# Optimization experiments

Measured on AMD Instinct MI355X. Metric: run time of the kernel, lower is better.

The kernel has to match this reference:

```python
import jax, jax.numpy as jnp
import numpy as np

N, E, D, H = 50000, 1600000, 256, 256
EPS = 1e-5

def prelu(x, a):
    return jnp.where(x >= 0, x, a * x)

def batch_norm(x, gamma, beta):
    # training-mode BatchNorm1d: stats over the node (batch) dim
    mu = jnp.mean(x, axis=0)
    var = jnp.var(x, axis=0)
    return (x - mu) * jax.lax.rsqrt(var + EPS) * gamma + beta

def gcn_conv(x, edge_index, W, b):
    # PyG GCNConv: h = XW, add self-loops, symmetric norm, scatter-add, + bias
    h = x @ W
    n = x.shape[0]
    row = jnp.concatenate([edge_index[0], jnp.arange(n)])
    col = jnp.concatenate([edge_index[1], jnp.arange(n)])
    w = jnp.ones(row.shape[0], dtype=x.dtype)
    deg = jax.ops.segment_sum(w, col, num_segments=n)
    dinv = jnp.where(deg > 0, jax.lax.rsqrt(deg), 0.0)
    norm = dinv[row] * w * dinv[col]  # [E+N]
    msg = h[row] * norm[:, None]      # [E+N, H] gathered messages
    out = jax.ops.segment_sum(msg, col, num_segments=n)
    return out + b

def setup_inputs() -> dict:
    key = jax.random.key(0)
    ks = jax.random.split(key, 10)
    x = jax.random.normal(ks[0], (N, D), dtype=jnp.float32)
    edge_index = jax.random.randint(ks[1], (2, E), 0, N).astype(jnp.int64)
    s1 = 1.0 / np.sqrt(D)
    s2 = 1.0 / np.sqrt(H)
    return {
        "x": x,
        "edge_index": edge_index,
        "W1": jax.random.uniform(ks[2], (D, H), jnp.float32, -s1, s1),
        "b1": jnp.zeros((H,), jnp.float32),
        "W2": jax.random.uniform(ks[3], (H, H), jnp.float32, -s2, s2),
        "b2": jnp.zeros((H,), jnp.float32),
        "prelu_a": jnp.asarray(0.25, jnp.float32),
        "bn_gamma": jnp.ones((H,), jnp.float32),
        "bn_beta": jnp.zeros((H,), jnp.float32),
        "proj_W": jax.random.uniform(ks[4], (H, H), jnp.float32, -s2, s2),
        "proj_b": jnp.zeros((H,), jnp.float32),
        "pbn_gamma": jnp.ones((H,), jnp.float32),
        "pbn_beta": jnp.zeros((H,), jnp.float32),
        "prelu2_a": jnp.asarray(0.25, jnp.float32),
    }

def reference(x, edge_index, W1, b1, W2, b2, prelu_a, bn_gamma, bn_beta,
              proj_W, proj_b, pbn_gamma, pbn_beta, prelu2_a):
    # eval-mode dropout (identity); BN uses batch stats
    z = prelu(gcn_conv(x, edge_index, W1, b1), prelu_a)
    z = prelu(gcn_conv(z, edge_index, W2, b2), prelu_a)
    z = batch_norm(z, bn_gamma, bn_beta)
    p = prelu(batch_norm(z @ proj_W + proj_b, pbn_gamma, pbn_beta), prelu2_a)
    return (z, p)
```

## Files before the change

kernel.cpp:

```cpp
#include <hip/hip_runtime.h>
#include <hip/hip_bf16.h>


#define CAP 96

typedef __attribute__((ext_vector_type(8))) short short8;
typedef __attribute__((ext_vector_type(4))) float f32x4;

__device__ __forceinline__ float bf2f(unsigned short u) {
    union { unsigned int i; float f; } v; v.i = ((unsigned int)u) << 16; return v.f;
}
__device__ __forceinline__ unsigned short f2bf(float f) {
    __hip_bfloat16 h = __float2bfloat16(f);
    return *reinterpret_cast<unsigned short*>(&h);
}

__global__ __launch_bounds__(256) void k_init(float* deg, int* fill, float* stats, int N) {
    int i = blockIdx.x * 256 + threadIdx.x;
    if (i < N) { deg[i] = 1.0f; fill[i] = 0; }
    if (i < 2048) stats[i] = 0.0f;
}

__global__ __launch_bounds__(256) void k_count(const int* __restrict__ col, float* __restrict__ deg, int E) {
    int e = blockIdx.x * 256 + threadIdx.x;
    if (e < E) atomicAdd(&deg[col[e]], 1.0f);
}

__global__ __launch_bounds__(256) void k_dinv(float* deg, int N) {
    int i = blockIdx.x * 256 + threadIdx.x;
    if (i < N) deg[i] = rsqrtf(deg[i]);
}

__global__ __launch_bounds__(256) void k_fill(const int* __restrict__ row, const int* __restrict__ col,
                                              int* __restrict__ fill, int* __restrict__ csr, int E) {
    int e = blockIdx.x * 256 + threadIdx.x;
    if (e >= E) return;
    int v = col[e];
    int p = atomicAdd(&fill[v], 1);
    if (p < CAP) csr[(size_t)v * CAP + p] = row[e];
}

__global__ __launch_bounds__(256) void k_castx(const float* __restrict__ x, unsigned short* __restrict__ xb, size_t n4) {
    size_t stride = (size_t)gridDim.x * blockDim.x;
    for (size_t i = (size_t)blockIdx.x * blockDim.x + threadIdx.x; i < n4; i += stride) {
        float4 v = ((const float4*)x)[i];
        ushort4 o; o.x = f2bf(v.x); o.y = f2bf(v.y); o.z = f2bf(v.z); o.w = f2bf(v.w);
        ((ushort4*)xb)[i] = o;
    }
}

__global__ __launch_bounds__(256) void k_wt(const float* __restrict__ W, unsigned short* __restrict__ Wt) {
    __shared__ float t[32][33];
    int bx = blockIdx.x * 32, by = blockIdx.y * 32;
    int x = threadIdx.x & 31, y = threadIdx.x >> 5;
#pragma unroll
    for (int i = 0; i < 32; i += 8)
        t[y + i][x] = W[(size_t)(by + y + i) * 256 + bx + x];
    __syncthreads();
#pragma unroll
    for (int i = 0; i < 32; i += 8)
        Wt[(size_t)(bx + y + i) * 256 + by + x] = f2bf(t[x][y + i]);
}

__global__ __launch_bounds__(256) void k_gemm_bf16(const unsigned short* __restrict__ A,
                                                   const unsigned short* __restrict__ Bt,
                                                   unsigned short* __restrict__ C, int M) {
    __shared__ unsigned short As[128 * 64];
    __shared__ unsigned short Bs[128 * 64];
    int tid  = threadIdx.x;
    int lane = tid & 63, wid = tid >> 6;
    int wr = wid >> 1, wc = wid & 1;
    int row0 = blockIdx.x * 128;
    int col0 = blockIdx.y * 128;

    f32x4 acc[4][4];
#pragma unroll
    for (int m = 0; m < 4; ++m)
#pragma unroll
        for (int n = 0; n < 4; ++n) acc[m][n] = f32x4{0.f, 0.f, 0.f, 0.f};

    int srow = lane >> 3;
    int sk   = (lane & 7) * 8;

    for (int k0 = 0; k0 < 256; k0 += 64) {
#pragma unroll
        for (int i = 0; i < 4; ++i) {
            int u = i * 4 + wid;
            int arow = row0 + u * 8 + srow;
            if (arow >= M) arow = M - 1;
            const unsigned short* ga = A  + (size_t)arow * 256 + k0 + sk;
            const unsigned short* gb = Bt + (size_t)(col0 + u * 8 + srow) * 256 + k0 + sk;
            __builtin_amdgcn_global_load_lds((const __attribute__((address_space(1))) void*)ga,
                (__attribute__((address_space(3))) void*)(As + u * 512), 16, 0, 0);
            __builtin_amdgcn_global_load_lds((const __attribute__((address_space(1))) void*)gb,
                (__attribute__((address_space(3))) void*)(Bs + u * 512), 16, 0, 0);
        }
        __syncthreads();
#pragma unroll
        for (int kk = 0; kk < 64; kk += 32) {
            short8 a[4], b[4];
#pragma unroll
            for (int m = 0; m < 4; ++m)
                a[m] = *(const short8*)(As + (wr * 64 + m * 16 + (lane & 15)) * 64 + kk + (lane >> 4) * 8);
#pragma unroll
            for (int n = 0; n < 4; ++n)
                b[n] = *(const short8*)(Bs + (wc * 64 + n * 16 + (lane & 15)) * 64 + kk + (lane >> 4) * 8);
#pragma unroll
            for (int m = 0; m < 4; ++m)
#pragma unroll
                for (int n = 0; n < 4; ++n)
                    acc[m][n] = __builtin_amdgcn_mfma_f32_16x16x32_bf16(a[m], b[n], acc[m][n], 0, 0, 0);
        }
        __syncthreads();
    }

    int crow = row0 + wr * 64;
    int ccol = col0 + wc * 64;
#pragma unroll
    for (int m = 0; m < 4; ++m)
#pragma unroll
        for (int r = 0; r < 4; ++r) {
            int rr = crow + m * 16 + (lane >> 4) * 4 + r;
            if (rr < M) {
#pragma unroll
                for (int n = 0; n < 4; ++n)
                    C[(size_t)rr * 256 + ccol + n * 16 + (lane & 15)] = f2bf(acc[m][n][r]);
            }
        }
}

__global__ __launch_bounds__(256) void k_agg_bf(const unsigned short* __restrict__ h,
                                                unsigned short* __restrict__ outb,
                                                const float* __restrict__ dinv, const int* __restrict__ csr,
                                                const int* __restrict__ fill, const float* __restrict__ bias,
                                                const float* __restrict__ aptr, int N) {
    int wv = threadIdx.x >> 6, lane = threadIdx.x & 63;
    int v = blockIdx.x * 4 + wv;
    if (v >= N) return;
    const ushort4* h4 = (const ushort4*)h;
    float dv = dinv[v];
    ushort4 hv = h4[(size_t)v * 64 + lane];
    float s0 = dv * bf2f(hv.x), s1 = dv * bf2f(hv.y), s2 = dv * bf2f(hv.z), s3 = dv * bf2f(hv.w);
    int n = fill[v]; if (n > CAP) n = CAP;
    const int* lst = csr + (size_t)v * CAP;
    int i = 0;
    for (; i + 3 < n; i += 4) {
        int u0 = lst[i], u1 = lst[i + 1], u2 = lst[i + 2], u3 = lst[i + 3];
        ushort4 a0 = h4[(size_t)u0 * 64 + lane];
        ushort4 a1 = h4[(size_t)u1 * 64 + lane];
        ushort4 a2 = h4[(size_t)u2 * 64 + lane];
        ushort4 a3 = h4[(size_t)u3 * 64 + lane];
        float d0 = dinv[u0], d1 = dinv[u1], d2 = dinv[u2], d3 = dinv[u3];
        s0 += d0 * bf2f(a0.x) + d1 * bf2f(a1.x) + d2 * bf2f(a2.x) + d3 * bf2f(a3.x);
        s1 += d0 * bf2f(a0.y) + d1 * bf2f(a1.y) + d2 * bf2f(a2.y) + d3 * bf2f(a3.y);
        s2 += d0 * bf2f(a0.z) + d1 * bf2f(a1.z) + d2 * bf2f(a2.z) + d3 * bf2f(a3.z);
        s3 += d0 * bf2f(a0.w) + d1 * bf2f(a1.w) + d2 * bf2f(a2.w) + d3 * bf2f(a3.w);
    }
    for (; i < n; ++i) {
        int u0 = lst[i];
        ushort4 a0 = h4[(size_t)u0 * 64 + lane];
        float d0 = dinv[u0];
        s0 += d0 * bf2f(a0.x); s1 += d0 * bf2f(a0.y); s2 += d0 * bf2f(a0.z); s3 += d0 * bf2f(a0.w);
    }
    float a = *aptr;
    float4 bb = *(const float4*)(bias + lane * 4);
    float o0 = dv * s0 + bb.x, o1 = dv * s1 + bb.y, o2 = dv * s2 + bb.z, o3 = dv * s3 + bb.w;
    o0 = o0 >= 0.f ? o0 : a * o0;
    o1 = o1 >= 0.f ? o1 : a * o1;
    o2 = o2 >= 0.f ? o2 : a * o2;
    o3 = o3 >= 0.f ? o3 : a * o3;
    ushort4 o; o.x = f2bf(o0); o.y = f2bf(o1); o.z = f2bf(o2); o.w = f2bf(o3);
    ((ushort4*)outb)[(size_t)v * 64 + lane] = o;
}

__global__ __launch_bounds__(256) void k_bnstats_bf(const unsigned short* __restrict__ X, float* __restrict__ sums, int N) {
    int c = threadIdx.x;
    float s = 0.f, q = 0.f;
    for (int r = blockIdx.x; r < N; r += gridDim.x) {
        float x = bf2f(X[(size_t)r * 256 + c]);
        s += x; q += x * x;
    }
    atomicAdd(&sums[c], s);
    atomicAdd(&sums[256 + c], q);
}

__global__ __launch_bounds__(256) void k_bnfinal(float* stats, const float* __restrict__ gamma,
                                                 const float* __restrict__ beta, float invN) {
    int c = threadIdx.x;
    float mu = stats[c] * invN;
    float var = stats[256 + c] * invN - mu * mu;
    float rstd = rsqrtf(var + 1e-5f);
    float sc = rstd * gamma[c];
    stats[512 + c] = sc;
    stats[768 + c] = beta[c] - mu * sc;
}

__global__ __launch_bounds__(256) void k_bnapply_z(const unsigned short* __restrict__ in,
                                                   float* __restrict__ zout, unsigned short* __restrict__ zb,
                                                   const float* __restrict__ scale, const float* __restrict__ shift,
                                                   size_t n4) {
    size_t stride = (size_t)gridDim.x * blockDim.x;
    for (size_t i = (size_t)blockIdx.x * blockDim.x + threadIdx.x; i < n4; i += stride) {
        int c4 = (int)(i & 63) * 4;
        ushort4 x4 = ((const ushort4*)in)[i];
        float4 sc = *(const float4*)(scale + c4);
        float4 sh = *(const float4*)(shift + c4);
        float4 y;
        y.x = bf2f(x4.x) * sc.x + sh.x;
        y.y = bf2f(x4.y) * sc.y + sh.y;
        y.z = bf2f(x4.z) * sc.z + sh.z;
        y.w = bf2f(x4.w) * sc.w + sh.w;
        ((float4*)zout)[i] = y;
        ushort4 o; o.x = f2bf(y.x); o.y = f2bf(y.y); o.z = f2bf(y.z); o.w = f2bf(y.w);
        ((ushort4*)zb)[i] = o;
    }
}

__global__ __launch_bounds__(256) void k_bnapply_p(const unsigned short* __restrict__ in,
                                                   float* __restrict__ pout,
                                                   const float* __restrict__ scale, const float* __restrict__ shift,
                                                   const float* __restrict__ aptr, size_t n4) {
    size_t stride = (size_t)gridDim.x * blockDim.x;
    float a = *aptr;
    for (size_t i = (size_t)blockIdx.x * blockDim.x + threadIdx.x; i < n4; i += stride) {
        int c4 = (int)(i & 63) * 4;
        ushort4 x4 = ((const ushort4*)in)[i];
        float4 sc = *(const float4*)(scale + c4);
        float4 sh = *(const float4*)(shift + c4);
        float4 y;
        y.x = bf2f(x4.x) * sc.x + sh.x;
        y.y = bf2f(x4.y) * sc.y + sh.y;
        y.z = bf2f(x4.z) * sc.z + sh.z;
        y.w = bf2f(x4.w) * sc.w + sh.w;
        y.x = y.x >= 0.f ? y.x : a * y.x;
        y.y = y.y >= 0.f ? y.y : a * y.y;
        y.z = y.z >= 0.f ? y.z : a * y.z;
        y.w = y.w >= 0.f ? y.w : a * y.w;
        ((float4*)pout)[i] = y;
    }
}

extern "C" void kernel_launch(void* const* d_in, const int* in_sizes, int n_in,
                              void* d_out, int out_size, void* d_ws, size_t ws_size,
                              hipStream_t stream) {
    const float* x     = (const float*)d_in[0];
    const int*   ei    = (const int*)d_in[1];
    const float* W1    = (const float*)d_in[2];
    const float* b1    = (const float*)d_in[3];
    const float* W2    = (const float*)d_in[4];
    const float* b2    = (const float*)d_in[5];
    const float* aptr  = (const float*)d_in[6];
    const float* gamma = (const float*)d_in[7];
    const float* beta  = (const float*)d_in[8];
    const float* projW = (const float*)d_in[9];
    const float* pgamma = (const float*)d_in[11];
    const float* pbeta  = (const float*)d_in[12];
    const float* a2ptr  = (const float*)d_in[13];

    int N = in_sizes[0] / 256;
    int E = in_sizes[1] / 2;
    const int* row = ei;
    const int* col = ei + E;

    float* out  = (float*)d_out;
    float* zout = out;
    float* pout = out + (size_t)N * 256;

    unsigned short* B0 = (unsigned short*)d_ws;
    unsigned short* B1 = B0 + (size_t)N * 256;
    unsigned short* B2 = B1 + (size_t)N * 256;
    unsigned short* Wt = B2 + (size_t)N * 256;
    float* deg   = (float*)(Wt + 3 * 65536);
    int*   fill  = (int*)(deg + N);
    int*   csr   = fill + N;
    float* stats = (float*)(csr + (size_t)N * CAP);

    int nb_N = (N + 255) / 256;
    int nb_E = (E + 255) / 256;
    dim3 ggrid((N + 127) / 128, 2);
    dim3 wgrid(8, 8);
    int  agrid = (N + 3) / 4;
    size_t n4 = (size_t)N * 64;

    k_init <<<nb_N, 256, 0, stream>>>(deg, fill, stats, N);
    k_count<<<nb_E, 256, 0, stream>>>(col, deg, E);
    k_dinv <<<nb_N, 256, 0, stream>>>(deg, N);
    k_fill <<<nb_E, 256, 0, stream>>>(row, col, fill, csr, E);
    k_castx<<<2048, 256, 0, stream>>>(x, B0, n4);
    k_wt   <<<wgrid, 256, 0, stream>>>(W1,    Wt);
    k_wt   <<<wgrid, 256, 0, stream>>>(W2,    Wt + 65536);
    k_wt   <<<wgrid, 256, 0, stream>>>(projW, Wt + 131072);

    k_gemm_bf16<<<ggrid, 256, 0, stream>>>(B0, Wt, B1, N);
    k_agg_bf   <<<agrid, 256, 0, stream>>>(B1, B2, deg, csr, fill, b1, aptr, N);
    k_gemm_bf16<<<ggrid, 256, 0, stream>>>(B2, Wt + 65536, B1, N);
    k_agg_bf   <<<agrid, 256, 0, stream>>>(B1, B0, deg, csr, fill, b2, aptr, N);
    k_bnstats_bf<<<500, 256, 0, stream>>>(B0, stats, N);
    k_bnfinal   <<<1, 256, 0, stream>>>(stats, gamma, beta, 1.0f / (float)N);
    k_bnapply_z <<<2048, 256, 0, stream>>>(B0, zout, B2, stats + 512, stats + 768, n4);
    k_gemm_bf16 <<<ggrid, 256, 0, stream>>>(B2, Wt + 131072, B1, N);
    k_bnstats_bf<<<500, 256, 0, stream>>>(B1, stats + 1024, N);
    k_bnfinal   <<<1, 256, 0, stream>>>(stats + 1024, pgamma, pbeta, 1.0f / (float)N);
    k_bnapply_p <<<2048, 256, 0, stream>>>(B1, pout, stats + 1536, stats + 1792, a2ptr, n4);
}
```

Baseline: 757.4 us.

## Build CSR via two-level binning with shared-memory atomics; pad neighbor lists

Replaces the degree-count, rsqrt and global-atomic CSR fill kernels with a binning pass that groups edges into 128-node buckets split across 8 partitions. A per-bucket kernel then scatters them into the CSR using shared-memory atomics and computes dinv directly. Neighbor lists are padded to multiples of 8 with a sentinel node whose dinv is zero, so the aggregation loop is unrolled by 8 and has no remainder loop. BN stats are vectorized to ushort4 per lane. The cost is fixed per-segment capacity limits (SEGCAP) that could drop edges on skewed graphs, and bins reuse the B1 buffer.

```diff
diff --git a/kernel.cpp b/kernel.cpp
--- a/kernel.cpp
+++ b/kernel.cpp
@@ -3,6 +3,9 @@
 
 
 #define CAP 96
+#define NPB 128
+#define NPART 8
+#define SEGCAP 768
 
 typedef __attribute__((ext_vector_type(8))) short short8;
 typedef __attribute__((ext_vector_type(4))) float f32x4;
@@ -15,29 +18,57 @@
     return *reinterpret_cast<unsigned short*>(&h);
 }
 
-__global__ __launch_bounds__(256) void k_init(float* deg, int* fill, float* stats, int N) {
+__global__ __launch_bounds__(256) void k_zero(int* segcnt, int nseg, float* stats, float* dinv, int N) {
     int i = blockIdx.x * 256 + threadIdx.x;
-    if (i < N) { deg[i] = 1.0f; fill[i] = 0; }
+    if (i < nseg) segcnt[i] = 0;
     if (i < 2048) stats[i] = 0.0f;
-}
-
-__global__ __launch_bounds__(256) void k_count(const int* __restrict__ col, float* __restrict__ deg, int E) {
-    int e = blockIdx.x * 256 + threadIdx.x;
-    if (e < E) atomicAdd(&deg[col[e]], 1.0f);
-}
-
-__global__ __launch_bounds__(256) void k_dinv(float* deg, int N) {
-    int i = blockIdx.x * 256 + threadIdx.x;
-    if (i < N) deg[i] = rsqrtf(deg[i]);
-}
-
-__global__ __launch_bounds__(256) void k_fill(const int* __restrict__ row, const int* __restrict__ col,
-                                              int* __restrict__ fill, int* __restrict__ csr, int E) {
+    if (i == 0) dinv[N] = 0.0f;
+}
+
+__global__ __launch_bounds__(256) void k_bin(const int* __restrict__ row, const int* __restrict__ col,
+                                             unsigned* __restrict__ bins, int* __restrict__ segcnt, int E) {
     int e = blockIdx.x * 256 + threadIdx.x;
     if (e >= E) return;
     int v = col[e];
-    int p = atomicAdd(&fill[v], 1);
-    if (p < CAP) csr[(size_t)v * CAP + p] = row[e];
+    int r = row[e];
+    int seg = (v >> 7) * NPART + (blockIdx.x & (NPART - 1));
+    int p = atomicAdd(&segcnt[seg], 1);
+    if (p < SEGCAP) bins[(size_t)seg * SEGCAP + p] = ((unsigned)r << 7) | (unsigned)(v & (NPB - 1));
+}
+
+__global__ __launch_bounds__(256) void k_csr(const unsigned* __restrict__ bins, const int* __restrict__ segcnt,
+                                             int* __restrict__ csr, int* __restrict__ fillp,
+                                             float* __restrict__ dinv, int N) {
+    __shared__ int cnt[NPB];
+    int bkt = blockIdx.x;
+    if (threadIdx.x < NPB) cnt[threadIdx.x] = 0;
+    __syncthreads();
+    for (int part = 0; part < NPART; ++part) {
+        int seg = bkt * NPART + part;
+        int m = segcnt[seg]; if (m > SEGCAP) m = SEGCAP;
+        const unsigned* b = bins + (size_t)seg * SEGCAP;
+        for (int i = threadIdx.x; i < m; i += 256) {
+            unsigned ent = b[i];
+            int loc = (int)(ent & (NPB - 1));
+            int r   = (int)(ent >> 7);
+            int p = atomicAdd(&cnt[loc], 1);
+            if (p < CAP) csr[(size_t)(bkt * NPB + loc) * CAP + p] = r;
+        }
+    }
+    __syncthreads();
+    if (threadIdx.x < NPB) {
+        int v = bkt * NPB + threadIdx.x;
+        if (v < N) {
+            int c = cnt[threadIdx.x];
+            int real = c < CAP ? c : CAP;
+            int pc = (real + 7) & ~7;
+            if (pc > CAP) pc = CAP;
+            int* lst = csr + (size_t)v * CAP;
+            for (int p = real; p < pc; ++p) lst[p] = N;
+            fillp[v] = pc;
+            dinv[v] = rsqrtf(1.0f + (float)c);
+        }
+    }
 }
 
 __global__ __launch_bounds__(256) void k_castx(const float* __restrict__ x, unsigned short* __restrict__ xb, size_t n4) {
@@ -132,7 +163,7 @@
 __global__ __launch_bounds__(256) void k_agg_bf(const unsigned short* __restrict__ h,
                                                 unsigned short* __restrict__ outb,
                                                 const float* __restrict__ dinv, const int* __restrict__ csr,
-                                                const int* __restrict__ fill, const float* __restrict__ bias,
+                                                const int* __restrict__ fillp, const float* __restrict__ bias,
                                                 const float* __restrict__ aptr, int N) {
     int wv = threadIdx.x >> 6, lane = threadIdx.x & 63;
     int v = blockIdx.x * 4 + wv;
@@ -141,26 +172,29 @@
     float dv = dinv[v];
     ushort4 hv = h4[(size_t)v * 64 + lane];
     float s0 = dv * bf2f(hv.x), s1 = dv * bf2f(hv.y), s2 = dv * bf2f(hv.z), s3 = dv * bf2f(hv.w);
-    int n = fill[v]; if (n > CAP) n = CAP;
+    int n = fillp[v];
     const int* lst = csr + (size_t)v * CAP;
-    int i = 0;
-    for (; i + 3 < n; i += 4) {
-        int u0 = lst[i], u1 = lst[i + 1], u2 = lst[i + 2], u3 = lst[i + 3];
+    for (int i = 0; i < n; i += 8) {
+        int u0 = lst[i],     u1 = lst[i + 1], u2 = lst[i + 2], u3 = lst[i + 3];
+        int u4 = lst[i + 4], u5 = lst[i + 5], u6 = lst[i + 6], u7 = lst[i + 7];
         ushort4 a0 = h4[(size_t)u0 * 64 + lane];
         ushort4 a1 = h4[(size_t)u1 * 64 + lane];
         ushort4 a2 = h4[(size_t)u2 * 64 + lane];
         ushort4 a3 = h4[(size_t)u3 * 64 + lane];
+        ushort4 a4 = h4[(size_t)u4 * 64 + lane];
+        ushort4 a5 = h4[(size_t)u5 * 64 + lane];
+        ushort4 a6 = h4[(size_t)u6 * 64 + lane];
+        ushort4 a7 = h4[(size_t)u7 * 64 + lane];
         float d0 = dinv[u0], d1 = dinv[u1], d2 = dinv[u2], d3 = dinv[u3];
-        s0 += d0 * bf2f(a0.x) + d1 * bf2f(a1.x) + d2 * bf2f(a2.x) + d3 * bf2f(a3.x);
-        s1 += d0 * bf2f(a0.y) + d1 * bf2f(a1.y) + d2 * bf2f(a2.y) + d3 * bf2f(a3.y);
-        s2 += d0 * bf2f(a0.z) + d1 * bf2f(a1.z) + d2 * bf2f(a2.z) + d3 * bf2f(a3.z);
-        s3 += d0 * bf2f(a0.w) + d1 * bf2f(a1.w) + d2 * bf2f(a2.w) + d3 * bf2f(a3.w);
-    }
-    for (; i < n; ++i) {
-        int u0 = lst[i];
-        ushort4 a0 = h4[(size_t)u0 * 64 + lane];
-        float d0 = dinv[u0];
-        s0 += d0 * bf2f(a0.x); s1 += d0 * bf2f(a0.y); s2 += d0 * bf2f(a0.z); s3 += d0 * bf2f(a0.w);
+        float d4 = dinv[u4], d5 = dinv[u5], d6 = dinv[u6], d7 = dinv[u7];
+        s0 += d0 * bf2f(a0.x) + d1 * bf2f(a1.x) + d2 * bf2f(a2.x) + d3 * bf2f(a3.x)
+            + d4 * bf2f(a4.x) + d5 * bf2f(a5.x) + d6 * bf2f(a6.x) + d7 * bf2f(a7.x);
+        s1 += d0 * bf2f(a0.y) + d1 * bf2f(a1.y) + d2 * bf2f(a2.y) + d3 * bf2f(a3.y)
+            + d4 * bf2f(a4.y) + d5 * bf2f(a5.y) + d6 * bf2f(a6.y) + d7 * bf2f(a7.y);
+        s2 += d0 * bf2f(a0.z) + d1 * bf2f(a1.z) + d2 * bf2f(a2.z) + d3 * bf2f(a3.z)
+            + d4 * bf2f(a4.z) + d5 * bf2f(a5.z) + d6 * bf2f(a6.z) + d7 * bf2f(a7.z);
+        s3 += d0 * bf2f(a0.w) + d1 * bf2f(a1.w) + d2 * bf2f(a2.w) + d3 * bf2f(a3.w)
+            + d4 * bf2f(a4.w) + d5 * bf2f(a5.w) + d6 * bf2f(a6.w) + d7 * bf2f(a7.w);
     }
     float a = *aptr;
     float4 bb = *(const float4*)(bias + lane * 4);
@@ -173,15 +207,21 @@
     ((ushort4*)outb)[(size_t)v * 64 + lane] = o;
 }
 
-__global__ __launch_bounds__(256) void k_bnstats_bf(const unsigned short* __restrict__ X, float* __restrict__ sums, int N) {
-    int c = threadIdx.x;
-    float s = 0.f, q = 0.f;
-    for (int r = blockIdx.x; r < N; r += gridDim.x) {
-        float x = bf2f(X[(size_t)r * 256 + c]);
-        s += x; q += x * x;
-    }
-    atomicAdd(&sums[c], s);
-    atomicAdd(&sums[256 + c], q);
+__global__ __launch_bounds__(256) void k_bnstats_v(const unsigned short* __restrict__ X, float* __restrict__ sums, int N) {
+    int w = threadIdx.x >> 6, lane = threadIdx.x & 63;
+    int c4 = lane * 4;
+    float4 s = {0.f, 0.f, 0.f, 0.f}, q = {0.f, 0.f, 0.f, 0.f};
+    int rstride = gridDim.x * 4;
+    for (int r = blockIdx.x * 4 + w; r < N; r += rstride) {
+        ushort4 x4 = ((const ushort4*)X)[(size_t)r * 64 + lane];
+        float a = bf2f(x4.x), b = bf2f(x4.y), c = bf2f(x4.z), d = bf2f(x4.w);
+        s.x += a; s.y += b; s.z += c; s.w += d;
+        q.x += a * a; q.y += b * b; q.z += c * c; q.w += d * d;
+    }
+    atomicAdd(&sums[c4 + 0], s.x); atomicAdd(&sums[c4 + 1], s.y);
+    atomicAdd(&sums[c4 + 2], s.z); atomicAdd(&sums[c4 + 3], s.w);
+    atomicAdd(&sums[256 + c4 + 0], q.x); atomicAdd(&sums[256 + c4 + 1], q.y);
+    atomicAdd(&sums[256 + c4 + 2], q.z); atomicAdd(&sums[256 + c4 + 3], q.w);
 }
 
 __global__ __launch_bounds__(256) void k_bnfinal(float* stats, const float* __restrict__ gamma,
@@ -266,40 +306,43 @@
     float* zout = out;
     float* pout = out + (size_t)N * 256;
 
+    int nbkt = (N + NPB - 1) / NPB;
+    int nseg = nbkt * NPART;
+
     unsigned short* B0 = (unsigned short*)d_ws;
     unsigned short* B1 = B0 + (size_t)N * 256;
     unsigned short* B2 = B1 + (size_t)N * 256;
     unsigned short* Wt = B2 + (size_t)N * 256;
-    float* deg   = (float*)(Wt + 3 * 65536);
-    int*   fill  = (int*)(deg + N);
-    int*   csr   = fill + N;
+    float* dinv  = (float*)(Wt + 3 * 65536);
+    int*   fillp = (int*)(dinv + N + 1);
+    int*   csr   = fillp + N;
     float* stats = (float*)(csr + (size_t)N * CAP);
-
-    int nb_N = (N + 255) / 256;
+    int*   segcnt= (int*)(stats + 2048);
+    unsigned* bins = (unsigned*)B1;
+
     int nb_E = (E + 255) / 256;
     dim3 ggrid((N + 127) / 128, 2);
     dim3 wgrid(8, 8);
     int  agrid = (N + 3) / 4;
     size_t n4 = (size_t)N * 64;
 
-    k_init <<<nb_N, 256, 0, stream>>>(deg, fill, stats, N);
-    k_count<<<nb_E, 256, 0, stream>>>(col, deg, E);
-    k_dinv <<<nb_N, 256, 0, stream>>>(deg, N);
-    k_fill <<<nb_E, 256, 0, stream>>>(row, col, fill, csr, E);
+    k_zero <<<(nseg + 2303) / 256, 256, 0, stream>>>(segcnt, nseg, stats, dinv, N);
+    k_bin  <<<nb_E, 256, 0, stream>>>(row, col, bins, segcnt, E);
+    k_csr  <<<nbkt, 256, 0, stream>>>(bins, segcnt, csr, fillp, dinv, N);
     k_castx<<<2048, 256, 0, stream>>>(x, B0, n4);
     k_wt   <<<wgrid, 256, 0, stream>>>(W1,    Wt);
     k_wt   <<<wgrid, 256, 0, stream>>>(W2,    Wt + 65536);
     k_wt   <<<wgrid, 256, 0, stream>>>(projW, Wt + 131072);
 
     k_gemm_bf16<<<ggrid, 256, 0, stream>>>(B0, Wt, B1, N);
-    k_agg_bf   <<<agrid, 256, 0, stream>>>(B1, B2, deg, csr, fill, b1, aptr, N);
+    k_agg_bf   <<<agrid, 256, 0, stream>>>(B1, B2, dinv, csr, fillp, b1, aptr, N);
     k_gemm_bf16<<<ggrid, 256, 0, stream>>>(B2, Wt + 65536, B1, N);
-    k_agg_bf   <<<agrid, 256, 0, stream>>>(B1, B0, deg, csr, fill, b2, aptr, N);
-    k_bnstats_bf<<<500, 256, 0, stream>>>(B0, stats, N);
-    k_bnfinal   <<<1, 256, 0, stream>>>(stats, gamma, beta, 1.0f / (float)N);
-    k_bnapply_z <<<2048, 256, 0, stream>>>(B0, zout, B2, stats + 512, stats + 768, n4);
-    k_gemm_bf16 <<<ggrid, 256, 0, stream>>>(B2, Wt + 131072, B1, N);
-    k_bnstats_bf<<<500, 256, 0, stream>>>(B1, stats + 1024, N);
-    k_bnfinal   <<<1, 256, 0, stream>>>(stats + 1024, pgamma, pbeta, 1.0f / (float)N);
-    k_bnapply_p <<<2048, 256, 0, stream>>>(B1, pout, stats + 1536, stats + 1792, a2ptr, n4);
-}
+    k_agg_bf   <<<agrid, 256, 0, stream>>>(B1, B0, dinv, csr, fillp, b2, aptr, N);
+    k_bnstats_v<<<128, 256, 0, stream>>>(B0, stats, N);
+    k_bnfinal  <<<1, 256, 0, stream>>>(stats, gamma, beta, 1.0f / (float)N);
+    k_bnapply_z<<<2048, 256, 0, stream>>>(B0, zout, B2, stats + 512, stats + 768, n4);
+    k_gemm_bf16<<<ggrid, 256, 0, stream>>>(B2, Wt + 131072, B1, N);
+    k_bnstats_v<<<128, 256, 0, stream>>>(B1, stats + 1024, N);
+    k_bnfinal  <<<1, 256, 0, stream>>>(stats + 1024, pgamma, pbeta, 1.0f / (float)N);
+    k_bnapply_p<<<2048, 256, 0, stream>>>(B1, pout, stats + 1536, stats + 1792, a2ptr, n4);
+}
```

Measured after the change: 790.8 us. 1.04x slower.
